# Optimization experiments

Hardware: AMD Instinct MI355X
Metric: run time of the kernel (lower is better)

Reference implementation:

```python
import jax, jax.numpy as jnp
import numpy as np

H = 8   # no_heads
D = 32  # c_hidden per head


def setup_inputs() -> dict:
    key = jax.random.key(0)
    ks = jax.random.split(key, 8)
    B, Q, K, C = 4, 1024, 1024, 256
    s = 0.02
    return {
        "q_x": jax.random.normal(ks[0], (B, Q, C), jnp.float32),
        "kv_x": jax.random.normal(ks[1], (B, K, C), jnp.float32),
        "mask_bias": jnp.zeros((B, 1, 1, K), jnp.float32),
        "pair_bias": jax.random.normal(ks[2], (B, H, Q, K), jnp.float32),
        "wq": jax.random.normal(ks[3], (H * D, C), jnp.float32) * s,
        "wk": jax.random.normal(ks[4], (H * D, C), jnp.float32) * s,
        "wv": jax.random.normal(ks[5], (H * D, C), jnp.float32) * s,
        "wg": jax.random.normal(ks[6], (H * D, C), jnp.float32) * s,
        "bg": jnp.zeros((H * D,), jnp.float32),
        "wo": jax.random.normal(ks[7], (C, H * D), jnp.float32) * s,
        "bo": jnp.zeros((C,), jnp.float32),
    }


def reference(q_x, kv_x, mask_bias, pair_bias, wq, wk, wv, wg, bg, wo, bo):
    B, Q, _ = q_x.shape
    K = kv_x.shape[1]
    # linear projections (no bias on q/k/v, as in OpenFold Attention)
    q = (q_x @ wq.T).reshape(B, Q, H, D) / jnp.sqrt(jnp.asarray(D, q_x.dtype))
    k = (kv_x @ wk.T).reshape(B, K, H, D)
    v = (kv_x @ wv.T).reshape(B, K, H, D)
    # scores + biases (mask bias broadcasts over heads/queries)
    a = jnp.einsum("bqhd,bkhd->bhqk", q, k) + mask_bias + pair_bias
    a = jax.nn.softmax(a, axis=-1)
    o = jnp.einsum("bhqk,bkhd->bqhd", a, v)  # [B,Q,H,D]
    # multiplicative gating from the query input
    g = jax.nn.sigmoid(q_x @ wg.T + bg).reshape(B, Q, H, D)
    o = o * g
    return (o.reshape(B, Q, H * D)) @ wo.T + bo
```

## Files before the change

### kernel.cpp

```cpp
#include <hip/hip_runtime.h>
#include <cstdint>
#include <cstddef>

typedef short bf16x8 __attribute__((ext_vector_type(8)));
typedef float f32x4 __attribute__((ext_vector_type(4)));
typedef unsigned short u16x4 __attribute__((ext_vector_type(4)));
typedef unsigned short u16x8 __attribute__((ext_vector_type(8)));

#define MFMA(a,b,c) __builtin_amdgcn_mfma_f32_16x16x32_bf16((a),(b),(c),0,0,0)

__device__ __forceinline__ unsigned short f2bf(float x){
  union { float f; unsigned u; } v; v.f = x;
  unsigned r = v.u + 0x7FFFu + ((v.u >> 16) & 1u);
  return (unsigned short)(r >> 16);
}
__device__ __forceinline__ float bf2f(unsigned short b){
  union { unsigned u; float f; } v; v.u = ((unsigned)b) << 16;
  return v.f;
}
__device__ __forceinline__ bf16x8 cvtld8(const float* p){
  f32x4 a = *(const f32x4*)p;
  f32x4 b = *(const f32x4*)(p + 4);
  bf16x8 r;
  r[0]=(short)f2bf(a.x); r[1]=(short)f2bf(a.y);
  r[2]=(short)f2bf(a.z); r[3]=(short)f2bf(a.w);
  r[4]=(short)f2bf(b.x); r[5]=(short)f2bf(b.y);
  r[6]=(short)f2bf(b.z); r[7]=(short)f2bf(b.w);
  return r;
}

__global__ __launch_bounds__(256) void wcvt_kernel(
    const float* __restrict__ wq, const float* __restrict__ wk,
    const float* __restrict__ wv, const float* __restrict__ wg,
    const float* __restrict__ wo, unsigned short* __restrict__ dst)
{
  const int which = blockIdx.x >> 5;
  const float* s = (which==0)?wq:(which==1)?wk:(which==2)?wv:(which==3)?wg:wo;
  const int off = (blockIdx.x & 31) * 2048 + threadIdx.x * 8;
  f32x4 a = *(const f32x4*)(s + off);
  f32x4 b = *(const f32x4*)(s + off + 4);
  u16x8 r;
  r[0]=f2bf(a.x); r[1]=f2bf(a.y); r[2]=f2bf(a.z); r[3]=f2bf(a.w);
  r[4]=f2bf(b.x); r[5]=f2bf(b.y); r[6]=f2bf(b.z); r[7]=f2bf(b.w);
  *(u16x8*)(dst + (size_t)which*65536 + off) = r;
}

__global__ __launch_bounds__(256,2) void proj_kernel(
    const float* __restrict__ q_x, const float* __restrict__ kv_x,
    const unsigned short* __restrict__ wb,
    const float* __restrict__ bg,
    unsigned short* __restrict__ qws, unsigned short* __restrict__ kws,
    unsigned short* __restrict__ vTws, unsigned short* __restrict__ gws)
{
  const int tid = threadIdx.x;
  const int w = tid >> 6, lane = tid & 63;
  const int c = lane & 15, qd = lane >> 4;
  const int side = blockIdx.x >> 8;
  const int rb = (blockIdx.x & 255) * 16;
  const float* X = side ? kv_x : q_x;
  const unsigned short* W0 = wb + (size_t)(side ? 1 : 0) * 65536;
  const unsigned short* W1 = wb + (size_t)(side ? 2 : 3) * 65536;
  const int hdw = w * 64;

  const f32x4 fz = {0.f,0.f,0.f,0.f};
  f32x4 acc[2][4];
  #pragma unroll
  for (int o=0;o<2;o++)
    #pragma unroll
    for (int mt=0;mt<4;mt++) acc[o][mt] = fz;

  #pragma unroll
  for (int ks = 0; ks < 8; ks++){
    const int ko = ks*32 + qd*8;
    bf16x8 bfrag = cvtld8(X + (size_t)(rb + c)*256 + ko);
    #pragma unroll
    for (int mt = 0; mt < 4; mt++){
      const int hd = hdw + mt*16 + c;
      bf16x8 a0 = *(const bf16x8*)(W0 + (size_t)hd*256 + ko);
      bf16x8 a1 = *(const bf16x8*)(W1 + (size_t)hd*256 + ko);
      acc[0][mt] = MFMA(a0, bfrag, acc[0][mt]);
      acc[1][mt] = MFMA(a1, bfrag, acc[1][mt]);
    }
  }

  const int row = rb + c;
  const int b = row >> 10, rr = row & 1023;
  #pragma unroll
  for (int mt = 0; mt < 4; mt++){
    const int hd0 = hdw + mt*16 + qd*4;
    const int h = hd0 >> 5, d0 = hd0 & 31;
    f32x4 v0 = acc[0][mt], v1 = acc[1][mt];
    if (side == 0){
      const float qs = 0.17677669529663687f;
      u16x4 oq = { f2bf(v0.x*qs), f2bf(v0.y*qs), f2bf(v0.z*qs), f2bf(v0.w*qs) };
      *(u16x4*)(qws + ((size_t)((b*8 + h)*1024 + rr))*32 + d0) = oq;
      f32x4 bg4 = *(const f32x4*)(bg + hd0);
      float g0 = 1.f/(1.f + exp2f(-1.44269504f*(v1.x + bg4.x)));
      float g1 = 1.f/(1.f + exp2f(-1.44269504f*(v1.y + bg4.y)));
      float g2 = 1.f/(1.f + exp2f(-1.44269504f*(v1.z + bg4.z)));
      float g3 = 1.f/(1.f + exp2f(-1.44269504f*(v1.w + bg4.w)));
      u16x4 og = { f2bf(g0), f2bf(g1), f2bf(g2), f2bf(g3) };
      *(u16x4*)(gws + ((size_t)((b*1024 + rr)*8 + h))*32 + d0) = og;
    } else {
      u16x4 ok = { f2bf(v0.x), f2bf(v0.y), f2bf(v0.z), f2bf(v0.w) };
      *(u16x4*)(kws + ((size_t)((b*8 + h)*1024 + rr))*32 + d0) = ok;
      size_t vb = ((size_t)((b*8 + h)*32 + d0))*1024 + rr;
      vTws[vb         ] = f2bf(v1.x);
      vTws[vb + 1024  ] = f2bf(v1.y);
      vTws[vb + 2048  ] = f2bf(v1.z);
      vTws[vb + 3072  ] = f2bf(v1.w);
    }
  }
}

__global__ __launch_bounds__(256,2) void attn_kernel(
    const float* __restrict__ pair_bias, const float* __restrict__ mask_bias,
    const unsigned short* __restrict__ qws, const unsigned short* __restrict__ kws,
    const unsigned short* __restrict__ vTws, const unsigned short* __restrict__ gws,
    unsigned short* __restrict__ ows)
{
  __shared__ __align__(16) unsigned short pT[4*4224];

  const int tid = threadIdx.x;
  const int w = tid >> 6, lane = tid & 63;
  const int c = lane & 15, qd = lane >> 4;
  const int bid = (int)((blockIdx.x & 7) * 64 + (blockIdx.x >> 3));
  const int bh = bid >> 4, qb = bid & 15;
  const int b  = bh >> 3, h = bh & 7;
  const int qrow = qb*64 + w*16 + c;

  const bf16x8 qf = *(const bf16x8*)(qws + ((size_t)bh*1024 + qrow)*32 + qd*8);
  const float* pbp = pair_bias + ((size_t)bh*1024 + qrow)*1024;
  const float* mbp = mask_bias + (size_t)b*1024;
  const unsigned short* kbp = kws  + (size_t)bh*32768;
  const unsigned short* vbp = vTws + (size_t)bh*32768;
  unsigned short* pTw = pT + w*4224;

  const f32x4 fz = {0.f,0.f,0.f,0.f};
  float m_i = -3.0e38f, l_i = 0.f;
  f32x4 accO0 = fz, accO1 = fz;

  #pragma unroll 1
  for (int kc = 0; kc < 4; kc++){
    const int k0 = kc*256;

    bf16x8 af[8]; f32x4 pb[8];
    #pragma unroll
    for (int i = 0; i < 8; i++){
      af[i] = *(const bf16x8*)(kbp + (size_t)(k0 + i*16 + c)*32 + qd*8);
      pb[i] = *(const f32x4*)(pbp + k0 + i*16 + qd*4);
    }
    f32x4 sf[16];
    float cmax = -3.0e38f;
    #pragma unroll
    for (int t = 0; t < 16; t++){
      const int r = t & 7;
      bf16x8 a   = af[r];
      f32x4 pbv  = pb[r];
      if (t < 8){
        af[r] = *(const bf16x8*)(kbp + (size_t)(k0 + (t+8)*16 + c)*32 + qd*8);
        pb[r] = *(const f32x4*)(pbp + k0 + (t+8)*16 + qd*4);
      }
      f32x4 mb = *(const f32x4*)(mbp + k0 + t*16 + qd*4);
      f32x4 s = MFMA(a, qf, fz);
      s = (s + pbv + mb) * 1.44269504f;
      sf[t] = s;
      cmax = fmaxf(cmax, fmaxf(fmaxf(s.x, s.y), fmaxf(s.z, s.w)));
    }
    cmax = fmaxf(cmax, __shfl_xor(cmax, 16));
    cmax = fmaxf(cmax, __shfl_xor(cmax, 32));
    const float m_new = fmaxf(m_i, cmax);
    const float alpha = exp2f(m_i - m_new);
    accO0 *= alpha; accO1 *= alpha;

    bf16x8 va0[8], va1[8];
    #pragma unroll
    for (int i = 0; i < 8; i++){
      va0[i] = *(const bf16x8*)(vbp + (size_t)c*1024      + k0 + i*32 + qd*8);
      va1[i] = *(const bf16x8*)(vbp + (size_t)(16+c)*1024 + k0 + i*32 + qd*8);
    }
    __builtin_amdgcn_sched_barrier(0);

    float rsum = 0.f;
    #pragma unroll
    for (int t = 0; t < 16; t++){
      f32x4 p;
      p.x = exp2f(sf[t].x - m_new);
      p.y = exp2f(sf[t].y - m_new);
      p.z = exp2f(sf[t].z - m_new);
      p.w = exp2f(sf[t].w - m_new);
      rsum += (p.x + p.y) + (p.z + p.w);
      u16x4 pk = { f2bf(p.x), f2bf(p.y), f2bf(p.z), f2bf(p.w) };
      *(u16x4*)(pTw + c*264 + t*16 + qd*4) = pk;
    }
    rsum += __shfl_xor(rsum, 16);
    rsum += __shfl_xor(rsum, 32);
    l_i = l_i*alpha + rsum;
    m_i = m_new;

    #pragma unroll
    for (int ks = 0; ks < 8; ks++){
      bf16x8 pf = *(const bf16x8*)(pTw + c*264 + ks*32 + qd*8);
      accO0 = MFMA(va0[ks], pf, accO0);
      accO1 = MFMA(va1[ks], pf, accO1);
    }
  }

  const float inv_l = 1.0f / l_i;
  const size_t obase = (((size_t)b*1024 + qrow)*8 + h)*32;
  {
    u16x4 g4 = *(const u16x4*)(gws + obase + qd*4);
    u16x4 o4 = { f2bf(accO0.x*inv_l*bf2f(g4[0])),
                 f2bf(accO0.y*inv_l*bf2f(g4[1])),
                 f2bf(accO0.z*inv_l*bf2f(g4[2])),
                 f2bf(accO0.w*inv_l*bf2f(g4[3])) };
    *(u16x4*)(ows + obase + qd*4) = o4;
  }
  {
    u16x4 g4 = *(const u16x4*)(gws + obase + 16 + qd*4);
    u16x4 o4 = { f2bf(accO1.x*inv_l*bf2f(g4[0])),
                 f2bf(accO1.y*inv_l*bf2f(g4[1])),
                 f2bf(accO1.z*inv_l*bf2f(g4[2])),
                 f2bf(accO1.w*inv_l*bf2f(g4[3])) };
    *(u16x4*)(ows + obase + 16 + qd*4) = o4;
  }
}

__global__ __launch_bounds__(256,2) void oproj_kernel(
    const unsigned short* __restrict__ ows, const unsigned short* __restrict__ wob,
    const float* __restrict__ bo, float* __restrict__ out)
{
  const int tid = threadIdx.x;
  const int w = tid >> 6, lane = tid & 63;
  const int c = lane & 15, qd = lane >> 4;
  const int row0 = blockIdx.x * 16;
  const int i0 = w * 64;

  const f32x4 fz = {0.f,0.f,0.f,0.f};
  f32x4 acc[4] = {fz, fz, fz, fz};
  #pragma unroll
  for (int ks = 0; ks < 8; ks++){
    const int ko = ks*32 + qd*8;
    bf16x8 bfrag = *(const bf16x8*)(ows + (size_t)(row0 + c)*256 + ko);
    #pragma unroll
    for (int mt = 0; mt < 4; mt++){
      bf16x8 afrag = *(const bf16x8*)(wob + (size_t)(i0 + mt*16 + c)*256 + ko);
      acc[mt] = MFMA(afrag, bfrag, acc[mt]);
    }
  }
  #pragma unroll
  for (int mt = 0; mt < 4; mt++){
    const int i = i0 + mt*16 + qd*4;
    f32x4 bo4 = *(const f32x4*)(bo + i);
    f32x4 r = acc[mt] + bo4;
    *(f32x4*)(out + (size_t)(row0 + c)*256 + i) = r;
  }
}

extern "C" void kernel_launch(void* const* d_in, const int* in_sizes, int n_in,
                              void* d_out, int out_size, void* d_ws, size_t ws_size,
                              hipStream_t stream) {
  const float* q_x       = (const float*)d_in[0];
  const float* kv_x      = (const float*)d_in[1];
  const float* mask_bias = (const float*)d_in[2];
  const float* pair_bias = (const float*)d_in[3];
  const float* wq        = (const float*)d_in[4];
  const float* wk        = (const float*)d_in[5];
  const float* wv        = (const float*)d_in[6];
  const float* wg        = (const float*)d_in[7];
  const float* bg        = (const float*)d_in[8];
  const float* wo        = (const float*)d_in[9];
  const float* bo        = (const float*)d_in[10];

  unsigned short* ws  = (unsigned short*)d_ws;
  unsigned short* qws  = ws;
  unsigned short* kws  = ws + (1u<<20);
  unsigned short* vTws = ws + 2*(1u<<20);
  unsigned short* gws  = ws + 3*(1u<<20);
  unsigned short* ows  = ws + 4*(1u<<20);
  unsigned short* wb   = ws + 5*(1u<<20);

  wcvt_kernel<<<160, 256, 0, stream>>>(wq, wk, wv, wg, wo, wb);
  proj_kernel<<<512, 256, 0, stream>>>(q_x, kv_x, wb, bg, qws, kws, vTws, gws);
  attn_kernel<<<512, 256, 0, stream>>>(pair_bias, mask_bias, qws, kws, vTws, gws, ows);
  oproj_kernel<<<256, 256, 0, stream>>>(ows, wb + 4*65536, bo, (float*)d_out);
}
```

Baseline: 273.3 us.

## Split attention key range across waves with LDS softmax merge

```diff
diff --git a/kernel.cpp b/kernel.cpp
--- a/kernel.cpp
+++ b/kernel.cpp
@@ -4,6 +4,7 @@
 
 typedef short bf16x8 __attribute__((ext_vector_type(8)));
 typedef float f32x4 __attribute__((ext_vector_type(4)));
+typedef unsigned short u16x2 __attribute__((ext_vector_type(2)));
 typedef unsigned short u16x4 __attribute__((ext_vector_type(4)));
 typedef unsigned short u16x8 __attribute__((ext_vector_type(8)));
 
@@ -113,7 +114,7 @@
   }
 }
 
-__global__ __launch_bounds__(256,2) void attn_kernel(
+__global__ __launch_bounds__(256,4) void attn_kernel(
     const float* __restrict__ pair_bias, const float* __restrict__ mask_bias,
     const unsigned short* __restrict__ qws, const unsigned short* __restrict__ kws,
     const unsigned short* __restrict__ vTws, const unsigned short* __restrict__ gws,
@@ -124,10 +125,11 @@
   const int tid = threadIdx.x;
   const int w = tid >> 6, lane = tid & 63;
   const int c = lane & 15, qd = lane >> 4;
-  const int bid = (int)((blockIdx.x & 7) * 64 + (blockIdx.x >> 3));
-  const int bh = bid >> 4, qb = bid & 15;
+  const int bid = (int)((blockIdx.x & 7) * 256 + (blockIdx.x >> 3));
+  const int bh = bid >> 6, qb16 = bid & 63;
   const int b  = bh >> 3, h = bh & 7;
-  const int qrow = qb*64 + w*16 + c;
+  const int qrow = qb16*16 + c;
+  const int k0 = w * 256;
 
   const bf16x8 qf = *(const bf16x8*)(qws + ((size_t)bh*1024 + qrow)*32 + qd*8);
   const float* pbp = pair_bias + ((size_t)bh*1024 + qrow)*1024;
@@ -137,93 +139,94 @@
   unsigned short* pTw = pT + w*4224;
 
   const f32x4 fz = {0.f,0.f,0.f,0.f};
-  float m_i = -3.0e38f, l_i = 0.f;
   f32x4 accO0 = fz, accO1 = fz;
 
-  #pragma unroll 1
-  for (int kc = 0; kc < 4; kc++){
-    const int k0 = kc*256;
-
-    bf16x8 af[8]; f32x4 pb[8];
-    #pragma unroll
-    for (int i = 0; i < 8; i++){
-      af[i] = *(const bf16x8*)(kbp + (size_t)(k0 + i*16 + c)*32 + qd*8);
-      pb[i] = *(const f32x4*)(pbp + k0 + i*16 + qd*4);
-    }
-    f32x4 sf[16];
-    float cmax = -3.0e38f;
-    #pragma unroll
-    for (int t = 0; t < 16; t++){
-      const int r = t & 7;
-      bf16x8 a   = af[r];
-      f32x4 pbv  = pb[r];
-      if (t < 8){
-        af[r] = *(const bf16x8*)(kbp + (size_t)(k0 + (t+8)*16 + c)*32 + qd*8);
-        pb[r] = *(const f32x4*)(pbp + k0 + (t+8)*16 + qd*4);
-      }
-      f32x4 mb = *(const f32x4*)(mbp + k0 + t*16 + qd*4);
-      f32x4 s = MFMA(a, qf, fz);
-      s = (s + pbv + mb) * 1.44269504f;
-      sf[t] = s;
-      cmax = fmaxf(cmax, fmaxf(fmaxf(s.x, s.y), fmaxf(s.z, s.w)));
-    }
-    cmax = fmaxf(cmax, __shfl_xor(cmax, 16));
-    cmax = fmaxf(cmax, __shfl_xor(cmax, 32));
-    const float m_new = fmaxf(m_i, cmax);
-    const float alpha = exp2f(m_i - m_new);
-    accO0 *= alpha; accO1 *= alpha;
-
-    bf16x8 va0[8], va1[8];
-    #pragma unroll
-    for (int i = 0; i < 8; i++){
-      va0[i] = *(const bf16x8*)(vbp + (size_t)c*1024      + k0 + i*32 + qd*8);
-      va1[i] = *(const bf16x8*)(vbp + (size_t)(16+c)*1024 + k0 + i*32 + qd*8);
-    }
-    __builtin_amdgcn_sched_barrier(0);
-
-    float rsum = 0.f;
-    #pragma unroll
-    for (int t = 0; t < 16; t++){
-      f32x4 p;
-      p.x = exp2f(sf[t].x - m_new);
-      p.y = exp2f(sf[t].y - m_new);
-      p.z = exp2f(sf[t].z - m_new);
-      p.w = exp2f(sf[t].w - m_new);
-      rsum += (p.x + p.y) + (p.z + p.w);
-      u16x4 pk = { f2bf(p.x), f2bf(p.y), f2bf(p.z), f2bf(p.w) };
-      *(u16x4*)(pTw + c*264 + t*16 + qd*4) = pk;
-    }
-    rsum += __shfl_xor(rsum, 16);
-    rsum += __shfl_xor(rsum, 32);
-    l_i = l_i*alpha + rsum;
-    m_i = m_new;
-
-    #pragma unroll
-    for (int ks = 0; ks < 8; ks++){
-      bf16x8 pf = *(const bf16x8*)(pTw + c*264 + ks*32 + qd*8);
-      accO0 = MFMA(va0[ks], pf, accO0);
-      accO1 = MFMA(va1[ks], pf, accO1);
-    }
-  }
-
-  const float inv_l = 1.0f / l_i;
-  const size_t obase = (((size_t)b*1024 + qrow)*8 + h)*32;
+  bf16x8 af[8]; f32x4 pb[8];
+  #pragma unroll
+  for (int i = 0; i < 8; i++){
+    af[i] = *(const bf16x8*)(kbp + (size_t)(k0 + i*16 + c)*32 + qd*8);
+    pb[i] = *(const f32x4*)(pbp + k0 + i*16 + qd*4);
+  }
+  f32x4 sf[16];
+  float cmax = -3.0e38f;
+  #pragma unroll
+  for (int t = 0; t < 16; t++){
+    const int r = t & 7;
+    bf16x8 a   = af[r];
+    f32x4 pbv  = pb[r];
+    if (t < 8){
+      af[r] = *(const bf16x8*)(kbp + (size_t)(k0 + (t+8)*16 + c)*32 + qd*8);
+      pb[r] = *(const f32x4*)(pbp + k0 + (t+8)*16 + qd*4);
+    }
+    f32x4 mb = *(const f32x4*)(mbp + k0 + t*16 + qd*4);
+    f32x4 s = MFMA(a, qf, fz);
+    s = (s + pbv + mb) * 1.44269504f;
+    sf[t] = s;
+    cmax = fmaxf(cmax, fmaxf(fmaxf(s.x, s.y), fmaxf(s.z, s.w)));
+  }
+  cmax = fmaxf(cmax, __shfl_xor(cmax, 16));
+  cmax = fmaxf(cmax, __shfl_xor(cmax, 32));
+  const float m_new = cmax;
+
+  bf16x8 va0[8], va1[8];
+  #pragma unroll
+  for (int i = 0; i < 8; i++){
+    va0[i] = *(const bf16x8*)(vbp + (size_t)c*1024      + k0 + i*32 + qd*8);
+    va1[i] = *(const bf16x8*)(vbp + (size_t)(16+c)*1024 + k0 + i*32 + qd*8);
+  }
+  __builtin_amdgcn_sched_barrier(0);
+
+  float rsum = 0.f;
+  #pragma unroll
+  for (int t = 0; t < 16; t++){
+    f32x4 p;
+    p.x = exp2f(sf[t].x - m_new);
+    p.y = exp2f(sf[t].y - m_new);
+    p.z = exp2f(sf[t].z - m_new);
+    p.w = exp2f(sf[t].w - m_new);
+    rsum += (p.x + p.y) + (p.z + p.w);
+    u16x4 pk = { f2bf(p.x), f2bf(p.y), f2bf(p.z), f2bf(p.w) };
+    *(u16x4*)(pTw + c*264 + t*16 + qd*4) = pk;
+  }
+  rsum += __shfl_xor(rsum, 16);
+  rsum += __shfl_xor(rsum, 32);
+
+  #pragma unroll
+  for (int ks = 0; ks < 8; ks++){
+    bf16x8 pf = *(const bf16x8*)(pTw + c*264 + ks*32 + qd*8);
+    accO0 = MFMA(va0[ks], pf, accO0);
+    accO1 = MFMA(va1[ks], pf, accO1);
+  }
+
+  __syncthreads();
+  float* mrg = (float*)pT;
+  if (qd == 0){
+    mrg[w*16 + c]      = m_new;
+    mrg[64 + w*16 + c] = rsum;
+  }
   {
-    u16x4 g4 = *(const u16x4*)(gws + obase + qd*4);
-    u16x4 o4 = { f2bf(accO0.x*inv_l*bf2f(g4[0])),
-                 f2bf(accO0.y*inv_l*bf2f(g4[1])),
-                 f2bf(accO0.z*inv_l*bf2f(g4[2])),
-                 f2bf(accO0.w*inv_l*bf2f(g4[3])) };
-    *(u16x4*)(ows + obase + qd*4) = o4;
-  }
-  {
-    u16x4 g4 = *(const u16x4*)(gws + obase + 16 + qd*4);
-    u16x4 o4 = { f2bf(accO1.x*inv_l*bf2f(g4[0])),
-                 f2bf(accO1.y*inv_l*bf2f(g4[1])),
-                 f2bf(accO1.z*inv_l*bf2f(g4[2])),
-                 f2bf(accO1.w*inv_l*bf2f(g4[3])) };
-    *(u16x4*)(ows + obase + 16 + qd*4) = o4;
-  }
+    float* Ow = mrg + 128 + w*512 + c*32;
+    *(f32x4*)(Ow + qd*4)      = accO0;
+    *(f32x4*)(Ow + 16 + qd*4) = accO1;
+  }
+  __syncthreads();
+
+  const int q  = tid >> 4;
+  const int d  = (tid & 15) * 2;
+  float m0 = mrg[q],      m1 = mrg[16 + q];
+  float m2 = mrg[32 + q], m3 = mrg[48 + q];
+  const float M = fmaxf(fmaxf(m0, m1), fmaxf(m2, m3));
+  const float w0 = exp2f(m0 - M), w1 = exp2f(m1 - M);
+  const float w2 = exp2f(m2 - M), w3 = exp2f(m3 - M);
+  const float L = mrg[64 + q]*w0 + mrg[80 + q]*w1 + mrg[96 + q]*w2 + mrg[112 + q]*w3;
+  const float* O0 = mrg + 128 + q*32 + d;
+  float oa = O0[0]*w0 + O0[512]*w1 + O0[1024]*w2 + O0[1536]*w3;
+  float ob = O0[1]*w0 + O0[513]*w1 + O0[1025]*w2 + O0[1537]*w3;
+  const float invL = 1.0f / L;
+  const size_t obase = (((size_t)b*1024 + qb16*16 + q)*8 + h)*32 + d;
+  u16x2 g2 = *(const u16x2*)(gws + obase);
+  u16x2 o2 = { f2bf(oa*invL*bf2f(g2[0])), f2bf(ob*invL*bf2f(g2[1])) };
+  *(u16x2*)(ows + obase) = o2;
 }
 
 __global__ __launch_bounds__(256,2) void oproj_kernel(
@@ -282,6 +285,7 @@
 
   wcvt_kernel<<<160, 256, 0, stream>>>(wq, wk, wv, wg, wo, wb);
   proj_kernel<<<512, 256, 0, stream>>>(q_x, kv_x, wb, bg, qws, kws, vTws, gws);
-  attn_kernel<<<512, 256, 0, stream>>>(pair_bias, mask_bias, qws, kws, vTws, gws, ows);
+  attn_kernel<<<2048, 256, 0, stream>>>(pair_bias, mask_bias, qws, kws, vTws,
+                                        gws, ows);
   oproj_kernel<<<256, 256, 0, stream>>>(ows, wb + 4*65536, bo, (float*)d_out);
 }
```

After: 287.9 us. +5.3%, slower.
